# Kernel tuning notes

Hardware: AMD Instinct MI355X
Metric: run time of the kernel (lower is better)

Reference implementation:

```python
import jax, jax.numpy as jnp
import numpy as np

# GNB per-element parameters [s, beta, R, C6] indexed by atomic number Z (rows not listed stay zero)
_ROWS = {
 1:[0.2772,1.7504,3.6516,95.99], 2:[0.2425,2.087,2.1843,40.67], 3:[0.3266,2.3073,1.2711,70.21],
 4:[0.3964,2.8811,3.3497,114.51], 5:[0.3121,2.6366,2.7079,152.36], 6:[0.2455,3.0189,1.8219,184.28],
 7:[0.2743,2.9432,2.4667,482.54], 8:[0.2577,2.7407,2.365,405.57], 9:[0.2791,2.5863,1.5062,218.45],
 10:[0.2378,2.5307,1.8233,174.81], 11:[0.2592,2.5679,1.3974,181.7], 12:[0.3837,2.9613,3.3515,263.02],
 13:[0.3013,3.2377,3.0102,228.1], 14:[0.3202,3.2749,3.1629,359.43], 15:[0.3399,3.7491,3.2554,3222.12],
 16:[0.3215,3.6718,2.9539,2144.49], 17:[0.3071,3.418,3.0368,2072.46], 18:[0.2752,3.3306,2.6598,1357.42],
 19:[0.2264,2.9736,4.0877,1406.65], 20:[0.4015,3.4464,4.1275,1058.36], 21:[0.9388,4.5955,9.7282,11498.73],
 22:[0.6048,3.5334,8.5322,3361.33], 23:[0.3678,3.068,7.2344,2095.91], 24:[0.2848,2.8393,5.3605,1049.31],
 25:[0.355,3.055,3.718,966.27], 26:[0.4406,3.2628,3.6408,1571.36], 27:[0.4124,3.2622,3.4961,1183.59],
 28:[0.3139,2.749,3.5108,787.76], 29:[0.3345,2.9097,3.0537,563.93], 30:[0.3391,2.9024,3.0261,592.91],
 31:[0.3146,3.3924,3.1735,430.82], 32:[0.3327,3.2804,3.1773,812.57], 33:[0.404,3.8757,3.8357,4533.53],
 34:[0.3343,3.8562,3.1109,3440.92], 35:[0.3242,3.7067,3.2122,3859.82], 36:[0.292,3.6457,2.8263,2729.6],
 37:[0.2677,3.4421,2.412,1864.19], 38:[0.3446,3.559,1.894,1175.73], 39:[1.0038,5.7293,11.2061,32141.18],
 40:[0.6146,5.075,6.821,27655.14], 41:[0.4244,3.7156,7.2367,2864.2], 42:[0.4882,3.6853,3.901,3563.45],
 43:[0.4439,3.6987,4.0857,3266.43], 44:[0.4736,3.7826,4.045,3967.23], 45:[0.4039,3.4706,3.4813,2233.82],
 46:[0.3188,3.3433,3.0487,1393.49], 47:[0.2948,3.1186,2.7795,1315.09], 48:[0.3012,3.0853,2.8673,1311.47],
 49:[0.3351,3.5452,3.3339,1460.56], 50:[0.3134,3.2997,3.0086,1662.99], 51:[0.4081,4.1277,3.9919,8089.97],
 52:[0.3585,4.1795,3.4209,6887.05], 53:[0.3574,4.0988,3.5649,8799.32], 54:[0.3134,4.0387,3.0288,6136.5],
 55:[0.2872,3.8468,2.262,3757.31], 56:[0.3788,4.0368,1.3837,2561.18], 57:[1.0851,6.1365,12.171,66580.83],
 72:[0.5577,5.213,6.0791,27593.76], 73:[0.5308,4.7637,5.7661,15364.65], 74:[0.3926,3.6018,3.6366,2734.5],
 75:[0.5351,3.9552,4.241,4801.82], 76:[0.4701,4.0278,4.1348,5685.94], 77:[0.3661,3.6123,3.4213,2786.0],
 78:[0.3411,3.6066,3.2486,2699.79], 79:[0.3164,3.3822,2.9588,2282.6], 80:[0.3047,3.375,2.9381,2476.79],
 81:[0.2802,3.3964,2.7711,2988.7], 82:[0.2682,3.2481,2.5816,2506.63], 83:[0.3876,4.1225,3.785,8916.84],
 84:[0.3679,4.2313,3.5381,8694.22], 85:[0.368,4.2455,3.6985,11821.61], 86:[0.3195,4.1784,3.0551,8410.64],
}
_TAB = np.zeros((87, 4), np.float32)
for _z, _v in _ROWS.items():
    _TAB[_z] = _v
GNB_TABLE = jnp.asarray(_TAB)
C_SP2 = jnp.asarray(np.array([0.2808, 3.0548, 2.2348, 429.69], np.float32))
C_SP3 = jnp.asarray(np.array([0.2455, 3.0189, 1.8219, 184.28], np.float32))
N_CN2 = jnp.asarray(np.array([0.2996, 3.02, 2.6454, 720.18], np.float32))
N_CN3 = jnp.asarray(np.array([0.2743, 2.9432, 2.4667, 482.54], np.float32))

BJ_A1, BJ_A2, BJ_ALPHA = 0.4, 4.0, 14.0
CUTOFF_LR, CUTOFF_START = 10.0, 8.0  # cutoff_start = cutoff_lr - 2.0


def _poly_envelope(x):
    # PolynomialCutoff.calculate_envelope with r_max=1, p=6:
    x6 = x ** 6
    env = 1.0 - 28.0 * x6 + 48.0 * x6 * x - 21.0 * x6 * x * x
    return env * (x < 1.0)


def _gnb_forward(lengths, Z, edge_index):
    n_nodes = Z.shape[0]
    sender, receiver = edge_index[0], edge_index[1]

    # coordination numbers via scatter-add on receiver
    cn = jnp.zeros((n_nodes,), jnp.int32).at[receiver].add(1)

    # species-indexed params with CN-adaptive selection for C and N
    params = GNB_TABLE[Z]  # [N, 4]
    c_params = jnp.where((cn <= 3)[:, None], C_SP2[None, :], C_SP3[None, :])
    n_params = jnp.where((cn <= 2)[:, None], N_CN2[None, :], N_CN3[None, :])
    params = jnp.where((Z == 6)[:, None], c_params, params)
    params = jnp.where((Z == 7)[:, None], n_params, params)

    R_i = params[:, 2]
    C6_i = params[:, 3]

    # geometric-mean combination rules per edge
    C6_ij = jnp.sqrt(C6_i[sender] * C6_i[receiver])
    R_ij = jnp.sqrt(R_i[sender] * R_i[receiver])

    r = lengths
    # BJ damping: f = 1 / (1 + 6 (r/r0)^(-alpha)), r0 = a1 sqrt(R_ij) + a2
    r0 = BJ_A1 * jnp.sqrt(R_ij) + BJ_A2
    f_damp = 1.0 / (1.0 + 6.0 * (r0 / r) ** BJ_ALPHA)

    e_edge = -C6_ij / (R_ij ** 6 + r ** 6) * f_damp

    # long-range polynomial cutoff switching from 1 at cutoff_start to 0 at cutoff_lr
    x = (r - CUTOFF_START) / (CUTOFF_LR - CUTOFF_START)
    env = jnp.where(r < CUTOFF_START, 1.0, _poly_envelope(x))
    e_edge = e_edge * env

    # scatter-sum to atoms; 0.5 to split symmetric pair energy over both directions
    node_energy = jnp.zeros((n_nodes,), e_edge.dtype).at[receiver].add(0.5 * e_edge)
    return node_energy


def setup_inputs() -> dict:
    key = jax.random.key(0)
    k1, k2, k3 = jax.random.split(key, 3)
    n_nodes, n_edges = 100000, 6400000
    Z = jax.random.randint(k1, (n_nodes,), 1, 87, dtype=jnp.int32)
    edge_index = jax.random.randint(k2, (2, n_edges), 0, n_nodes, dtype=jnp.int32)
    lengths = jax.random.uniform(k3, (n_edges,), jnp.float32, 1.0, 10.5)
    return {"Z": Z, "edge_index": edge_index, "lengths": lengths}


def reference(Z, edge_index, lengths):
    return _gnb_forward(lengths, Z, edge_index)
```

## Files before the change

### kernel.cpp

```cpp
#include <hip/hip_runtime.h>


#define B2SHIFT 10
#define B2SIZE  1024
#define TILE    4096
#define SBLK    512
#define ESLICES 32
#define MAXB    128

__device__ __constant__ float2 GNB_RC6[87] = {
    {0.f, 0.f},
    {3.6516f, 95.99f},   {2.1843f, 40.67f},   {1.2711f, 70.21f},
    {3.3497f, 114.51f},  {2.7079f, 152.36f},  {1.8219f, 184.28f},
    {2.4667f, 482.54f},  {2.365f, 405.57f},   {1.5062f, 218.45f},
    {1.8233f, 174.81f},  {1.3974f, 181.7f},   {3.3515f, 263.02f},
    {3.0102f, 228.1f},   {3.1629f, 359.43f},  {3.2554f, 3222.12f},
    {2.9539f, 2144.49f}, {3.0368f, 2072.46f}, {2.6598f, 1357.42f},
    {4.0877f, 1406.65f}, {4.1275f, 1058.36f}, {9.7282f, 11498.73f},
    {8.5322f, 3361.33f}, {7.2344f, 2095.91f}, {5.3605f, 1049.31f},
    {3.718f, 966.27f},   {3.6408f, 1571.36f}, {3.4961f, 1183.59f},
    {3.5108f, 787.76f},  {3.0537f, 563.93f},  {3.0261f, 592.91f},
    {3.1735f, 430.82f},  {3.1773f, 812.57f},  {3.8357f, 4533.53f},
    {3.1109f, 3440.92f}, {3.2122f, 3859.82f}, {2.8263f, 2729.6f},
    {2.412f, 1864.19f},  {1.894f, 1175.73f},  {11.2061f, 32141.18f},
    {6.821f, 27655.14f}, {7.2367f, 2864.2f},  {3.901f, 3563.45f},
    {4.0857f, 3266.43f}, {4.045f, 3967.23f},  {3.4813f, 2233.82f},
    {3.0487f, 1393.49f}, {2.7795f, 1315.09f}, {2.8673f, 1311.47f},
    {3.3339f, 1460.56f}, {3.0086f, 1662.99f}, {3.9919f, 8089.97f},
    {3.4209f, 6887.05f}, {3.5649f, 8799.32f}, {3.0288f, 6136.5f},
    {2.262f, 3757.31f},  {1.3837f, 2561.18f}, {12.171f, 66580.83f},
    {0.f,0.f},{0.f,0.f},{0.f,0.f},{0.f,0.f},{0.f,0.f},{0.f,0.f},{0.f,0.f},
    {0.f,0.f},{0.f,0.f},{0.f,0.f},{0.f,0.f},{0.f,0.f},{0.f,0.f},{0.f,0.f},
    {6.0791f, 27593.76f}, {5.7661f, 15364.65f}, {3.6366f, 2734.5f},
    {4.241f, 4801.82f},   {4.1348f, 5685.94f},  {3.4213f, 2786.0f},
    {3.2486f, 2699.79f},  {2.9588f, 2282.6f},   {2.9381f, 2476.79f},
    {2.7711f, 2988.7f},   {2.5816f, 2506.63f},  {3.785f, 8916.84f},
    {3.5381f, 8694.22f},  {3.6985f, 11821.61f}, {3.0551f, 8410.64f},
};

__global__ void gnb_init(const int* __restrict__ Z, unsigned* __restrict__ isCN,
                         int nw, int n_nodes, int* __restrict__ zp, int zwords) {
    int stride = gridDim.x * blockDim.x;
    int t0 = blockIdx.x * blockDim.x + threadIdx.x;
    for (int i = t0; i < zwords; i += stride) zp[i] = 0;
    for (int w = t0; w < nw; w += stride) {
        unsigned m = 0;
        int base = w << 5;
        int lim = n_nodes - base; if (lim > 32) lim = 32;
        for (int k = 0; k < lim; ++k) {
            int z = Z[base + k];
            if (z == 6 || z == 7) m |= (1u << k);
        }
        isCN[w] = m;
    }
}

__global__ void __launch_bounds__(SBLK)
gnb_scatter(const int* __restrict__ send, const int* __restrict__ recv,
            const float* __restrict__ len, const unsigned* __restrict__ isCN,
            int* __restrict__ cn,
            uint2* __restrict__ buckets, unsigned* __restrict__ cursor,
            uint4* __restrict__ ovrec, unsigned* __restrict__ ocur,
            int n_edges, int cap, unsigned ocap, int NB2) {
    __shared__ unsigned cnt[MAXB];
    __shared__ unsigned pos[MAXB];
    __shared__ unsigned startp[MAXB + 1];
    __shared__ unsigned gbase[MAXB];
    __shared__ uint2 srec[TILE];
    __shared__ unsigned char bmap[TILE];
    const int tid = threadIdx.x;
    const int e0  = blockIdx.x * TILE;

    for (int b = tid; b < MAXB; b += SBLK) { cnt[b] = 0; pos[b] = 0; }
    __syncthreads();

    #pragma unroll
    for (int k = 0; k < 2; ++k) {
        int base = e0 + (k * SBLK + tid) * 4;
        if (base + 3 < n_edges) {
            int4   rv = *(const int4*)(recv + base);
            float4 lv = *(const float4*)(len + base);
            int rr[4] = {rv.x, rv.y, rv.z, rv.w};
            float ll[4] = {lv.x, lv.y, lv.z, lv.w};
            #pragma unroll
            for (int j = 0; j < 4; ++j) {
                unsigned r = (unsigned)rr[j];
                if (ll[j] < 10.0f) atomicAdd(&cnt[r >> B2SHIFT], 1u);
                if ((isCN[r >> 5] >> (r & 31)) & 1u) atomicAdd(&cn[r], 1);
            }
        } else {
            int lim = n_edges - base; if (lim < 0) lim = 0; if (lim > 4) lim = 4;
            for (int j = 0; j < lim; ++j) {
                unsigned r = (unsigned)recv[base + j];
                if (len[base + j] < 10.0f) atomicAdd(&cnt[r >> B2SHIFT], 1u);
                if ((isCN[r >> 5] >> (r & 31)) & 1u) atomicAdd(&cn[r], 1);
            }
        }
    }
    __syncthreads();

    if (tid == 0) {
        unsigned acc = 0;
        for (int b = 0; b < NB2; ++b) { startp[b] = acc; acc += cnt[b]; }
        startp[NB2] = acc;
    }
    __syncthreads();
    if (tid < NB2) gbase[tid] = atomicAdd(&cursor[tid], cnt[tid]);
    __syncthreads();

    #pragma unroll
    for (int k = 0; k < 2; ++k) {
        int base = e0 + (k * SBLK + tid) * 4;
        if (base + 3 < n_edges) {
            int4   sv = *(const int4*)(send + base);
            int4   rv = *(const int4*)(recv + base);
            uint4  lv = *(const uint4*)(len + base);
            int ss[4] = {sv.x, sv.y, sv.z, sv.w};
            int rr[4] = {rv.x, rv.y, rv.z, rv.w};
            unsigned ll[4] = {lv.x, lv.y, lv.z, lv.w};
            #pragma unroll
            for (int j = 0; j < 4; ++j) {
                if (__uint_as_float(ll[j]) >= 10.0f) continue;
                unsigned r = (unsigned)rr[j];
                unsigned b = r >> B2SHIFT;
                unsigned slot = startp[b] + atomicAdd(&pos[b], 1u);
                srec[slot] = make_uint2((unsigned)ss[j] | ((r & (B2SIZE - 1)) << 17), ll[j]);
                bmap[slot] = (unsigned char)b;
            }
        } else {
            int lim = n_edges - base; if (lim < 0) lim = 0; if (lim > 4) lim = 4;
            for (int j = 0; j < lim; ++j) {
                unsigned lbits = ((const unsigned*)len)[base + j];
                if (__uint_as_float(lbits) >= 10.0f) continue;
                unsigned r = (unsigned)recv[base + j];
                unsigned b = r >> B2SHIFT;
                unsigned slot = startp[b] + atomicAdd(&pos[b], 1u);
                srec[slot] = make_uint2((unsigned)send[base + j] | ((r & (B2SIZE - 1)) << 17),
                                        lbits);
                bmap[slot] = (unsigned char)b;
            }
        }
    }
    __syncthreads();

    unsigned total = startp[NB2];
    for (unsigned i = tid; i < total; i += SBLK) {
        unsigned b = bmap[i];
        unsigned g = gbase[b] + (i - startp[b]);
        uint2 rec = srec[i];
        if (g < (unsigned)cap) {
            buckets[(size_t)b * cap + g] = rec;
        } else {
            unsigned o = atomicAdd(ocur, 1u);
            unsigned r = ((unsigned)b << B2SHIFT) | ((rec.x >> 17) & (B2SIZE - 1));
            if (o < ocap) ovrec[o] = make_uint4(r, rec.x & 0x1FFFFu, rec.y, 0u);
        }
    }
}

__global__ void gnb_params(const int* __restrict__ Z, const int* __restrict__ cn,
                           float2* __restrict__ P2, int n_nodes) {
    int i = blockIdx.x * blockDim.x + threadIdx.x;
    if (i >= n_nodes) return;
    int z = Z[i];
    float Rp, C6;
    if (z == 6) {
        if (cn[i] <= 3) { Rp = 2.2348f; C6 = 429.69f; }
        else            { Rp = 1.8219f; C6 = 184.28f; }
    } else if (z == 7) {
        if (cn[i] <= 2) { Rp = 2.6454f; C6 = 720.18f; }
        else            { Rp = 2.4667f; C6 = 482.54f; }
    } else {
        float2 rc = GNB_RC6[z];
        Rp = rc.x; C6 = rc.y;
    }
    P2[i] = make_float2(sqrtf(C6), sqrtf(sqrtf(Rp)));
}

__device__ __forceinline__ float gnb_energy_eval(float2 ps, float2 pr, float rlen) {
    float env;
    if (rlen < 8.0f) {
        env = 1.0f;
    } else {
        float x = (rlen - 8.0f) * 0.5f;
        float x2 = x * x;
        float x6 = x2 * x2 * x2;
        env = 1.0f - 28.0f * x6 + 48.0f * x6 * x - 21.0f * x6 * x2;
    }
    float sR  = ps.y * pr.y;
    float C6  = ps.x * pr.x;
    float Rij = sR * sR;
    float R3  = Rij * Rij * Rij;
    float R6  = R3 * R3;
    float r0  = 0.4f * sR + 4.0f;
    float t   = r0 / rlen;
    float t2 = t * t, t4 = t2 * t2, t8 = t4 * t4;
    float t14 = t8 * t4 * t2;
    float fd = 1.0f / (1.0f + 6.0f * t14);
    float rl2 = rlen * rlen;
    float r6 = rl2 * rl2 * rl2;
    return -0.5f * C6 / (R6 + r6) * fd * env;
}

__global__ void __launch_bounds__(256)
gnb_energy(const uint2* __restrict__ buckets, const unsigned* __restrict__ cursor,
           const float2* __restrict__ P2, float* __restrict__ rep,
           int cap, int n_nodes) {
    __shared__ float  acc[2][B2SIZE + 8];
    __shared__ float2 p2loc[B2SIZE];
    const int b   = blockIdx.x / ESLICES;
    const int sl  = blockIdx.x % ESLICES;
    const int tid = threadIdx.x;
    const int rr  = (tid >> 6) & 1;

    for (int i = tid; i < 2 * (B2SIZE + 8); i += 256) acc[0][i] = 0.0f;
    for (int i = tid; i < B2SIZE; i += 256) {
        int node = (b << B2SHIFT) + i;
        p2loc[i] = (node < n_nodes) ? P2[node] : make_float2(0.f, 0.f);
    }
    __syncthreads();

    unsigned count = cursor[b];
    if (count > (unsigned)cap) count = (unsigned)cap;
    unsigned seg = (count + ESLICES - 1) / ESLICES;
    unsigned st  = (unsigned)sl * seg;
    unsigned en  = st + seg; if (en > count) en = count;

    const uint2* src = buckets + (size_t)b * cap;
    for (unsigned i = st + tid; i < en; i += 256) {
        uint2 rec = src[i];
        unsigned s    = rec.x & 0x1FFFFu;
        unsigned rlow = (rec.x >> 17) & (B2SIZE - 1);
        float e = gnb_energy_eval(P2[s], p2loc[rlow], __uint_as_float(rec.y));
        atomicAdd(&acc[rr][rlow], e);
    }
    __syncthreads();

    float* dst = rep + (size_t)blockIdx.x * B2SIZE;
    for (int i = tid; i < B2SIZE; i += 256) dst[i] = acc[0][i] + acc[1][i];
}

__global__ void gnb_ovf_energy(const uint4* __restrict__ ovrec, const unsigned* __restrict__ ocur,
                               const float2* __restrict__ P2, float* __restrict__ ovf,
                               unsigned ocap) {
    unsigned n = *ocur; if (n > ocap) n = ocap;
    int stride = gridDim.x * blockDim.x;
    for (unsigned i = blockIdx.x * blockDim.x + threadIdx.x; i < n; i += stride) {
        uint4 rec = ovrec[i];
        float rlen = __uint_as_float(rec.z);
        if (rlen >= 10.0f) continue;
        float e = gnb_energy_eval(P2[rec.y], P2[rec.x], rlen);
        atomicAdd(&ovf[rec.x], e);
    }
}

__global__ void gnb_reduce(const float* __restrict__ rep, const float* __restrict__ ovf,
                           float* __restrict__ out, int n_nodes) {
    int i = blockIdx.x * blockDim.x + threadIdx.x;
    if (i >= n_nodes) return;
    int b = i >> B2SHIFT;
    int j = i & (B2SIZE - 1);
    const float* src = rep + ((size_t)b * ESLICES) * B2SIZE + j;
    float sum = ovf[i];
    #pragma unroll
    for (int s = 0; s < ESLICES; ++s) sum += src[(size_t)s * B2SIZE];
    out[i] = sum;
}

extern "C" void kernel_launch(void* const* d_in, const int* in_sizes, int n_in,
                              void* d_out, int out_size, void* d_ws, size_t ws_size,
                              hipStream_t stream) {
    const int*   Z    = (const int*)d_in[0];
    const int*   eidx = (const int*)d_in[1];
    const float* len  = (const float*)d_in[2];
    float*       out  = (float*)d_out;

    const int n_nodes = in_sizes[0];
    const int n_edges = in_sizes[2];
    const int* send = eidx;
    const int* recv = eidx + n_edges;

    const int NB2 = (n_nodes + B2SIZE - 1) >> B2SHIFT;
    const int nw  = (n_nodes + 31) >> 5;
    const int nwp = (nw + 7) & ~7;

    char* ws = (char*)d_ws;
    unsigned* cursor = (unsigned*)ws;
    unsigned* ocur   = (unsigned*)(ws + MAXB * 4);
    int*      cn     = (int*)(ws + (MAXB + 8) * 4);
    float*    ovf    = (float*)(ws + ((size_t)n_nodes + MAXB + 8) * 4);
    float2*   P2     = (float2*)(ws + ((size_t)2 * n_nodes + MAXB + 8) * 4);
    unsigned* isCN   = (unsigned*)(ws + ((size_t)4 * n_nodes + MAXB + 8) * 4);
    float*    rep    = (float*)((char*)isCN + (size_t)nwp * 4);
    size_t rep_w     = (size_t)NB2 * ESLICES * B2SIZE;
    char*     tail   = (char*)rep + rep_w * 4;

    size_t fixed_words = (size_t)4 * n_nodes + MAXB + 8 + nwp + rep_w;
    size_t total_words = ws_size / 4;
    size_t avail = total_words > fixed_words ? total_words - fixed_words : 0;
    size_t ovw = avail / 32;
    unsigned ocap = (unsigned)(ovw / 4);
    long cap = (long)((avail - ovw) / (2 * (size_t)NB2));
    if (cap > n_edges) cap = n_edges;
    if (cap < 0) cap = 0;
    uint4* ovrec   = (uint4*)tail;
    uint2* buckets = (uint2*)(tail + (size_t)ocap * 16);

    const int B = 256;
    int node_blocks = (n_nodes + B - 1) / B;
    int scat_blocks = (n_edges + TILE - 1) / TILE;
    int zero_words  = 2 * n_nodes + MAXB + 8;

    gnb_init<<<256, B, 0, stream>>>(Z, isCN, nw, n_nodes, (int*)ws, zero_words);
    gnb_scatter<<<scat_blocks, SBLK, 0, stream>>>(send, recv, len, isCN, cn, buckets,
                                                  cursor, ovrec, ocur, n_edges,
                                                  (int)cap, ocap, NB2);
    gnb_params<<<node_blocks, B, 0, stream>>>(Z, cn, P2, n_nodes);
    gnb_energy<<<NB2 * ESLICES, B, 0, stream>>>(buckets, cursor, P2, rep, (int)cap, n_nodes);
    gnb_ovf_energy<<<8, B, 0, stream>>>(ovrec, ocur, P2, ovf, ocap);
    gnb_reduce<<<node_blocks, B, 0, stream>>>(rep, ovf, out, n_nodes);
}
```

Measured before the change: 202.4 us.

## Replace bucketed receiver sort with direct global atomics into replicated outputs

```diff
diff --git a/kernel.cpp b/kernel.cpp
--- a/kernel.cpp
+++ b/kernel.cpp
@@ -1,12 +1,8 @@
 #include <hip/hip_runtime.h>
 
 
-#define B2SHIFT 10
-#define B2SIZE  1024
-#define TILE    4096
-#define SBLK    512
-#define ESLICES 32
-#define MAXB    128
+#define REP 16
+#define EB  256
 
 __device__ __constant__ float2 GNB_RC6[87] = {
     {0.f, 0.f},
@@ -38,11 +34,22 @@
     {3.5381f, 8694.22f},  {3.6985f, 11821.61f}, {3.0551f, 8410.64f},
 };
 
+__device__ __forceinline__ void atomic_fadd(float* p, float v) {
+#if defined(__HIP_PLATFORM_AMD__)
+    unsafeAtomicAdd(p, v);
+#else
+    atomicAdd(p, v);
+#endif
+}
+
 __global__ void gnb_init(const int* __restrict__ Z, unsigned* __restrict__ isCN,
-                         int nw, int n_nodes, int* __restrict__ zp, int zwords) {
+                         int nw, int n_nodes, int4* __restrict__ zp4, int zq,
+                         int* __restrict__ zp, long zwords) {
     int stride = gridDim.x * blockDim.x;
     int t0 = blockIdx.x * blockDim.x + threadIdx.x;
-    for (int i = t0; i < zwords; i += stride) zp[i] = 0;
+    int4 z4 = make_int4(0, 0, 0, 0);
+    for (int i = t0; i < zq; i += stride) zp4[i] = z4;
+    for (long i = (long)zq * 4 + t0; i < zwords; i += stride) zp[i] = 0;
     for (int w = t0; w < nw; w += stride) {
         unsigned m = 0;
         int base = w << 5;
@@ -55,105 +62,25 @@
     }
 }
 
-__global__ void __launch_bounds__(SBLK)
-gnb_scatter(const int* __restrict__ send, const int* __restrict__ recv,
-            const float* __restrict__ len, const unsigned* __restrict__ isCN,
-            int* __restrict__ cn,
-            uint2* __restrict__ buckets, unsigned* __restrict__ cursor,
-            uint4* __restrict__ ovrec, unsigned* __restrict__ ocur,
-            int n_edges, int cap, unsigned ocap, int NB2) {
-    __shared__ unsigned cnt[MAXB];
-    __shared__ unsigned pos[MAXB];
-    __shared__ unsigned startp[MAXB + 1];
-    __shared__ unsigned gbase[MAXB];
-    __shared__ uint2 srec[TILE];
-    __shared__ unsigned char bmap[TILE];
-    const int tid = threadIdx.x;
-    const int e0  = blockIdx.x * TILE;
-
-    for (int b = tid; b < MAXB; b += SBLK) { cnt[b] = 0; pos[b] = 0; }
-    __syncthreads();
-
-    #pragma unroll
-    for (int k = 0; k < 2; ++k) {
-        int base = e0 + (k * SBLK + tid) * 4;
-        if (base + 3 < n_edges) {
-            int4   rv = *(const int4*)(recv + base);
-            float4 lv = *(const float4*)(len + base);
-            int rr[4] = {rv.x, rv.y, rv.z, rv.w};
-            float ll[4] = {lv.x, lv.y, lv.z, lv.w};
-            #pragma unroll
-            for (int j = 0; j < 4; ++j) {
-                unsigned r = (unsigned)rr[j];
-                if (ll[j] < 10.0f) atomicAdd(&cnt[r >> B2SHIFT], 1u);
+__global__ void __launch_bounds__(EB)
+gnb_degree(const int* __restrict__ recv, const unsigned* __restrict__ isCN,
+           int* __restrict__ cn, int n_edges) {
+    int base = (blockIdx.x * EB + threadIdx.x) * 4;
+    if (base + 3 < n_edges) {
+        int4 rv = *(const int4*)(recv + base);
+        int rr[4] = {rv.x, rv.y, rv.z, rv.w};
+        #pragma unroll
+        for (int j = 0; j < 4; ++j) {
+            unsigned r = (unsigned)rr[j];
+            if ((isCN[r >> 5] >> (r & 31)) & 1u) atomicAdd(&cn[r], 1);
+        }
+    } else {
+        for (int j = 0; j < 4; ++j) {
+            int e = base + j;
+            if (e < n_edges) {
+                unsigned r = (unsigned)recv[e];
                 if ((isCN[r >> 5] >> (r & 31)) & 1u) atomicAdd(&cn[r], 1);
             }
-        } else {
-            int lim = n_edges - base; if (lim < 0) lim = 0; if (lim > 4) lim = 4;
-            for (int j = 0; j < lim; ++j) {
-                unsigned r = (unsigned)recv[base + j];
-                if (len[base + j] < 10.0f) atomicAdd(&cnt[r >> B2SHIFT], 1u);
-                if ((isCN[r >> 5] >> (r & 31)) & 1u) atomicAdd(&cn[r], 1);
-            }
-        }
-    }
-    __syncthreads();
-
-    if (tid == 0) {
-        unsigned acc = 0;
-        for (int b = 0; b < NB2; ++b) { startp[b] = acc; acc += cnt[b]; }
-        startp[NB2] = acc;
-    }
-    __syncthreads();
-    if (tid < NB2) gbase[tid] = atomicAdd(&cursor[tid], cnt[tid]);
-    __syncthreads();
-
-    #pragma unroll
-    for (int k = 0; k < 2; ++k) {
-        int base = e0 + (k * SBLK + tid) * 4;
-        if (base + 3 < n_edges) {
-            int4   sv = *(const int4*)(send + base);
-            int4   rv = *(const int4*)(recv + base);
-            uint4  lv = *(const uint4*)(len + base);
-            int ss[4] = {sv.x, sv.y, sv.z, sv.w};
-            int rr[4] = {rv.x, rv.y, rv.z, rv.w};
-            unsigned ll[4] = {lv.x, lv.y, lv.z, lv.w};
-            #pragma unroll
-            for (int j = 0; j < 4; ++j) {
-                if (__uint_as_float(ll[j]) >= 10.0f) continue;
-                unsigned r = (unsigned)rr[j];
-                unsigned b = r >> B2SHIFT;
-                unsigned slot = startp[b] + atomicAdd(&pos[b], 1u);
-                srec[slot] = make_uint2((unsigned)ss[j] | ((r & (B2SIZE - 1)) << 17), ll[j]);
-                bmap[slot] = (unsigned char)b;
-            }
-        } else {
-            int lim = n_edges - base; if (lim < 0) lim = 0; if (lim > 4) lim = 4;
-            for (int j = 0; j < lim; ++j) {
-                unsigned lbits = ((const unsigned*)len)[base + j];
-                if (__uint_as_float(lbits) >= 10.0f) continue;
-                unsigned r = (unsigned)recv[base + j];
-                unsigned b = r >> B2SHIFT;
-                unsigned slot = startp[b] + atomicAdd(&pos[b], 1u);
-                srec[slot] = make_uint2((unsigned)send[base + j] | ((r & (B2SIZE - 1)) << 17),
-                                        lbits);
-                bmap[slot] = (unsigned char)b;
-            }
-        }
-    }
-    __syncthreads();
-
-    unsigned total = startp[NB2];
-    for (unsigned i = tid; i < total; i += SBLK) {
-        unsigned b = bmap[i];
-        unsigned g = gbase[b] + (i - startp[b]);
-        uint2 rec = srec[i];
-        if (g < (unsigned)cap) {
-            buckets[(size_t)b * cap + g] = rec;
-        } else {
-            unsigned o = atomicAdd(ocur, 1u);
-            unsigned r = ((unsigned)b << B2SHIFT) | ((rec.x >> 17) & (B2SIZE - 1));
-            if (o < ocap) ovrec[o] = make_uint4(r, rec.x & 0x1FFFFu, rec.y, 0u);
         }
     }
 }
@@ -202,69 +129,51 @@
     return -0.5f * C6 / (R6 + r6) * fd * env;
 }
 
-__global__ void __launch_bounds__(256)
-gnb_energy(const uint2* __restrict__ buckets, const unsigned* __restrict__ cursor,
-           const float2* __restrict__ P2, float* __restrict__ rep,
-           int cap, int n_nodes) {
-    __shared__ float  acc[2][B2SIZE + 8];
-    __shared__ float2 p2loc[B2SIZE];
-    const int b   = blockIdx.x / ESLICES;
-    const int sl  = blockIdx.x % ESLICES;
-    const int tid = threadIdx.x;
-    const int rr  = (tid >> 6) & 1;
-
-    for (int i = tid; i < 2 * (B2SIZE + 8); i += 256) acc[0][i] = 0.0f;
-    for (int i = tid; i < B2SIZE; i += 256) {
-        int node = (b << B2SHIFT) + i;
-        p2loc[i] = (node < n_nodes) ? P2[node] : make_float2(0.f, 0.f);
-    }
-    __syncthreads();
-
-    unsigned count = cursor[b];
-    if (count > (unsigned)cap) count = (unsigned)cap;
-    unsigned seg = (count + ESLICES - 1) / ESLICES;
-    unsigned st  = (unsigned)sl * seg;
-    unsigned en  = st + seg; if (en > count) en = count;
-
-    const uint2* src = buckets + (size_t)b * cap;
-    for (unsigned i = st + tid; i < en; i += 256) {
-        uint2 rec = src[i];
-        unsigned s    = rec.x & 0x1FFFFu;
-        unsigned rlow = (rec.x >> 17) & (B2SIZE - 1);
-        float e = gnb_energy_eval(P2[s], p2loc[rlow], __uint_as_float(rec.y));
-        atomicAdd(&acc[rr][rlow], e);
-    }
-    __syncthreads();
-
-    float* dst = rep + (size_t)blockIdx.x * B2SIZE;
-    for (int i = tid; i < B2SIZE; i += 256) dst[i] = acc[0][i] + acc[1][i];
-}
-
-__global__ void gnb_ovf_energy(const uint4* __restrict__ ovrec, const unsigned* __restrict__ ocur,
-                               const float2* __restrict__ P2, float* __restrict__ ovf,
-                               unsigned ocap) {
-    unsigned n = *ocur; if (n > ocap) n = ocap;
-    int stride = gridDim.x * blockDim.x;
-    for (unsigned i = blockIdx.x * blockDim.x + threadIdx.x; i < n; i += stride) {
-        uint4 rec = ovrec[i];
-        float rlen = __uint_as_float(rec.z);
-        if (rlen >= 10.0f) continue;
-        float e = gnb_energy_eval(P2[rec.y], P2[rec.x], rlen);
-        atomicAdd(&ovf[rec.x], e);
-    }
-}
-
-__global__ void gnb_reduce(const float* __restrict__ rep, const float* __restrict__ ovf,
-                           float* __restrict__ out, int n_nodes) {
+__global__ void __launch_bounds__(EB)
+gnb_energy(const int* __restrict__ send, const int* __restrict__ recv,
+           const float* __restrict__ len, const float2* __restrict__ P2,
+           float* __restrict__ outrep, int n_edges, int n_nodes) {
+    float* myout = outrep +
+        (size_t)(((blockIdx.x << 2) + (threadIdx.x >> 6)) & (REP - 1)) * n_nodes;
+    int base = (blockIdx.x * EB + threadIdx.x) * 4;
+    if (base + 3 < n_edges) {
+        int4   sv = *(const int4*)(send + base);
+        int4   rv = *(const int4*)(recv + base);
+        float4 lv = *(const float4*)(len + base);
+        int ss[4] = {sv.x, sv.y, sv.z, sv.w};
+        int rr[4] = {rv.x, rv.y, rv.z, rv.w};
+        float ll[4] = {lv.x, lv.y, lv.z, lv.w};
+        #pragma unroll
+        for (int j = 0; j < 4; ++j) {
+            if (ll[j] < 10.0f) {
+                float2 ps = P2[ss[j]];
+                float2 pr = P2[rr[j]];
+                float e = gnb_energy_eval(ps, pr, ll[j]);
+                atomic_fadd(&myout[rr[j]], e);
+            }
+        }
+    } else {
+        for (int j = 0; j < 4; ++j) {
+            int e = base + j;
+            if (e < n_edges) {
+                float l = len[e];
+                if (l < 10.0f) {
+                    float en = gnb_energy_eval(P2[send[e]], P2[recv[e]], l);
+                    atomic_fadd(&myout[recv[e]], en);
+                }
+            }
+        }
+    }
+}
+
+__global__ void gnb_reduce(const float* __restrict__ outrep, float* __restrict__ out,
+                           int n_nodes) {
     int i = blockIdx.x * blockDim.x + threadIdx.x;
     if (i >= n_nodes) return;
-    int b = i >> B2SHIFT;
-    int j = i & (B2SIZE - 1);
-    const float* src = rep + ((size_t)b * ESLICES) * B2SIZE + j;
-    float sum = ovf[i];
+    float s = 0.0f;
     #pragma unroll
-    for (int s = 0; s < ESLICES; ++s) sum += src[(size_t)s * B2SIZE];
-    out[i] = sum;
+    for (int rpl = 0; rpl < REP; ++rpl) s += outrep[(size_t)rpl * n_nodes + i];
+    out[i] = s;
 }
 
 extern "C" void kernel_launch(void* const* d_in, const int* in_sizes, int n_in,
@@ -280,43 +189,27 @@
     const int* send = eidx;
     const int* recv = eidx + n_edges;
 
-    const int NB2 = (n_nodes + B2SIZE - 1) >> B2SHIFT;
-    const int nw  = (n_nodes + 31) >> 5;
-    const int nwp = (nw + 7) & ~7;
+    const int nw = (n_nodes + 31) >> 5;
 
     char* ws = (char*)d_ws;
-    unsigned* cursor = (unsigned*)ws;
-    unsigned* ocur   = (unsigned*)(ws + MAXB * 4);
-    int*      cn     = (int*)(ws + (MAXB + 8) * 4);
-    float*    ovf    = (float*)(ws + ((size_t)n_nodes + MAXB + 8) * 4);
-    float2*   P2     = (float2*)(ws + ((size_t)2 * n_nodes + MAXB + 8) * 4);
-    unsigned* isCN   = (unsigned*)(ws + ((size_t)4 * n_nodes + MAXB + 8) * 4);
-    float*    rep    = (float*)((char*)isCN + (size_t)nwp * 4);
-    size_t rep_w     = (size_t)NB2 * ESLICES * B2SIZE;
-    char*     tail   = (char*)rep + rep_w * 4;
-
-    size_t fixed_words = (size_t)4 * n_nodes + MAXB + 8 + nwp + rep_w;
-    size_t total_words = ws_size / 4;
-    size_t avail = total_words > fixed_words ? total_words - fixed_words : 0;
-    size_t ovw = avail / 32;
-    unsigned ocap = (unsigned)(ovw / 4);
-    long cap = (long)((avail - ovw) / (2 * (size_t)NB2));
-    if (cap > n_edges) cap = n_edges;
-    if (cap < 0) cap = 0;
-    uint4* ovrec   = (uint4*)tail;
-    uint2* buckets = (uint2*)(tail + (size_t)ocap * 16);
+    int*      cn     = (int*)ws;
+    float*    outrep = (float*)(ws + (size_t)n_nodes * 4);
+    size_t    p2off  = (((size_t)(1 + REP) * n_nodes) + 1) & ~(size_t)1;
+    float2*   P2     = (float2*)(ws + p2off * 4);
+    unsigned* isCN   = (unsigned*)(ws + (p2off + (size_t)2 * n_nodes) * 4);
+
+    long zwords = (long)(1 + REP) * n_nodes;
+    int  zq     = (int)(zwords / 4);
 
     const int B = 256;
     int node_blocks = (n_nodes + B - 1) / B;
-    int scat_blocks = (n_edges + TILE - 1) / TILE;
-    int zero_words  = 2 * n_nodes + MAXB + 8;
-
-    gnb_init<<<256, B, 0, stream>>>(Z, isCN, nw, n_nodes, (int*)ws, zero_words);
-    gnb_scatter<<<scat_blocks, SBLK, 0, stream>>>(send, recv, len, isCN, cn, buckets,
-                                                  cursor, ovrec, ocur, n_edges,
-                                                  (int)cap, ocap, NB2);
+    int edge_blocks = (n_edges + EB * 4 - 1) / (EB * 4);
+
+    gnb_init<<<256, B, 0, stream>>>(Z, isCN, nw, n_nodes, (int4*)ws, zq,
+                                    (int*)ws, zwords);
+    gnb_degree<<<edge_blocks, EB, 0, stream>>>(recv, isCN, cn, n_edges);
     gnb_params<<<node_blocks, B, 0, stream>>>(Z, cn, P2, n_nodes);
-    gnb_energy<<<NB2 * ESLICES, B, 0, stream>>>(buckets, cursor, P2, rep, (int)cap, n_nodes);
-    gnb_ovf_energy<<<8, B, 0, stream>>>(ovrec, ocur, P2, ovf, ocap);
-    gnb_reduce<<<node_blocks, B, 0, stream>>>(rep, ovf, out, n_nodes);
-}
+    gnb_energy<<<edge_blocks, EB, 0, stream>>>(send, recv, len, P2, outrep,
+                                               n_edges, n_nodes);
+    gnb_reduce<<<node_blocks, B, 0, stream>>>(outrep, out, n_nodes);
+}
```

After: 409.5 us. 2.02x slower.

## Compute edge energies during scatter and bucket energies instead of sender/length records

Applied to the files above, without the earlier changes.

```diff
diff --git a/kernel.cpp b/kernel.cpp
--- a/kernel.cpp
+++ b/kernel.cpp
@@ -5,8 +5,10 @@
 #define B2SIZE  1024
 #define TILE    4096
 #define SBLK    512
+#define NWAVE   8
 #define ESLICES 32
 #define MAXB    128
+#define EB      256
 
 __device__ __constant__ float2 GNB_RC6[87] = {
     {0.f, 0.f},
@@ -38,11 +40,22 @@
     {3.5381f, 8694.22f},  {3.6985f, 11821.61f}, {3.0551f, 8410.64f},
 };
 
+__device__ __forceinline__ void atomic_fadd(float* p, float v) {
+#if defined(__HIP_PLATFORM_AMD__)
+    unsafeAtomicAdd(p, v);
+#else
+    atomicAdd(p, v);
+#endif
+}
+
 __global__ void gnb_init(const int* __restrict__ Z, unsigned* __restrict__ isCN,
-                         int nw, int n_nodes, int* __restrict__ zp, int zwords) {
+                         int nw, int n_nodes, int4* __restrict__ zp4, int zq,
+                         int* __restrict__ zp, int zwords) {
     int stride = gridDim.x * blockDim.x;
     int t0 = blockIdx.x * blockDim.x + threadIdx.x;
-    for (int i = t0; i < zwords; i += stride) zp[i] = 0;
+    int4 z4 = make_int4(0, 0, 0, 0);
+    for (int i = t0; i < zq; i += stride) zp4[i] = z4;
+    for (int i = zq * 4 + t0; i < zwords; i += stride) zp[i] = 0;
     for (int w = t0; w < nw; w += stride) {
         unsigned m = 0;
         int base = w << 5;
@@ -55,105 +68,25 @@
     }
 }
 
-__global__ void __launch_bounds__(SBLK)
-gnb_scatter(const int* __restrict__ send, const int* __restrict__ recv,
-            const float* __restrict__ len, const unsigned* __restrict__ isCN,
-            int* __restrict__ cn,
-            uint2* __restrict__ buckets, unsigned* __restrict__ cursor,
-            uint4* __restrict__ ovrec, unsigned* __restrict__ ocur,
-            int n_edges, int cap, unsigned ocap, int NB2) {
-    __shared__ unsigned cnt[MAXB];
-    __shared__ unsigned pos[MAXB];
-    __shared__ unsigned startp[MAXB + 1];
-    __shared__ unsigned gbase[MAXB];
-    __shared__ uint2 srec[TILE];
-    __shared__ unsigned char bmap[TILE];
-    const int tid = threadIdx.x;
-    const int e0  = blockIdx.x * TILE;
-
-    for (int b = tid; b < MAXB; b += SBLK) { cnt[b] = 0; pos[b] = 0; }
-    __syncthreads();
-
-    #pragma unroll
-    for (int k = 0; k < 2; ++k) {
-        int base = e0 + (k * SBLK + tid) * 4;
-        if (base + 3 < n_edges) {
-            int4   rv = *(const int4*)(recv + base);
-            float4 lv = *(const float4*)(len + base);
-            int rr[4] = {rv.x, rv.y, rv.z, rv.w};
-            float ll[4] = {lv.x, lv.y, lv.z, lv.w};
-            #pragma unroll
-            for (int j = 0; j < 4; ++j) {
-                unsigned r = (unsigned)rr[j];
-                if (ll[j] < 10.0f) atomicAdd(&cnt[r >> B2SHIFT], 1u);
+__global__ void __launch_bounds__(EB)
+gnb_degree(const int* __restrict__ recv, const unsigned* __restrict__ isCN,
+           int* __restrict__ cn, int n_edges) {
+    int base = (blockIdx.x * EB + threadIdx.x) * 4;
+    if (base + 3 < n_edges) {
+        int4 rv = *(const int4*)(recv + base);
+        int rr[4] = {rv.x, rv.y, rv.z, rv.w};
+        #pragma unroll
+        for (int j = 0; j < 4; ++j) {
+            unsigned r = (unsigned)rr[j];
+            if ((isCN[r >> 5] >> (r & 31)) & 1u) atomicAdd(&cn[r], 1);
+        }
+    } else {
+        for (int j = 0; j < 4; ++j) {
+            int e = base + j;
+            if (e < n_edges) {
+                unsigned r = (unsigned)recv[e];
                 if ((isCN[r >> 5] >> (r & 31)) & 1u) atomicAdd(&cn[r], 1);
             }
-        } else {
-            int lim = n_edges - base; if (lim < 0) lim = 0; if (lim > 4) lim = 4;
-            for (int j = 0; j < lim; ++j) {
-                unsigned r = (unsigned)recv[base + j];
-                if (len[base + j] < 10.0f) atomicAdd(&cnt[r >> B2SHIFT], 1u);
-                if ((isCN[r >> 5] >> (r & 31)) & 1u) atomicAdd(&cn[r], 1);
-            }
-        }
-    }
-    __syncthreads();
-
-    if (tid == 0) {
-        unsigned acc = 0;
-        for (int b = 0; b < NB2; ++b) { startp[b] = acc; acc += cnt[b]; }
-        startp[NB2] = acc;
-    }
-    __syncthreads();
-    if (tid < NB2) gbase[tid] = atomicAdd(&cursor[tid], cnt[tid]);
-    __syncthreads();
-
-    #pragma unroll
-    for (int k = 0; k < 2; ++k) {
-        int base = e0 + (k * SBLK + tid) * 4;
-        if (base + 3 < n_edges) {
-            int4   sv = *(const int4*)(send + base);
-            int4   rv = *(const int4*)(recv + base);
-            uint4  lv = *(const uint4*)(len + base);
-            int ss[4] = {sv.x, sv.y, sv.z, sv.w};
-            int rr[4] = {rv.x, rv.y, rv.z, rv.w};
-            unsigned ll[4] = {lv.x, lv.y, lv.z, lv.w};
-            #pragma unroll
-            for (int j = 0; j < 4; ++j) {
-                if (__uint_as_float(ll[j]) >= 10.0f) continue;
-                unsigned r = (unsigned)rr[j];
-                unsigned b = r >> B2SHIFT;
-                unsigned slot = startp[b] + atomicAdd(&pos[b], 1u);
-                srec[slot] = make_uint2((unsigned)ss[j] | ((r & (B2SIZE - 1)) << 17), ll[j]);
-                bmap[slot] = (unsigned char)b;
-            }
-        } else {
-            int lim = n_edges - base; if (lim < 0) lim = 0; if (lim > 4) lim = 4;
-            for (int j = 0; j < lim; ++j) {
-                unsigned lbits = ((const unsigned*)len)[base + j];
-                if (__uint_as_float(lbits) >= 10.0f) continue;
-                unsigned r = (unsigned)recv[base + j];
-                unsigned b = r >> B2SHIFT;
-                unsigned slot = startp[b] + atomicAdd(&pos[b], 1u);
-                srec[slot] = make_uint2((unsigned)send[base + j] | ((r & (B2SIZE - 1)) << 17),
-                                        lbits);
-                bmap[slot] = (unsigned char)b;
-            }
-        }
-    }
-    __syncthreads();
-
-    unsigned total = startp[NB2];
-    for (unsigned i = tid; i < total; i += SBLK) {
-        unsigned b = bmap[i];
-        unsigned g = gbase[b] + (i - startp[b]);
-        uint2 rec = srec[i];
-        if (g < (unsigned)cap) {
-            buckets[(size_t)b * cap + g] = rec;
-        } else {
-            unsigned o = atomicAdd(ocur, 1u);
-            unsigned r = ((unsigned)b << B2SHIFT) | ((rec.x >> 17) & (B2SIZE - 1));
-            if (o < ocap) ovrec[o] = make_uint4(r, rec.x & 0x1FFFFu, rec.y, 0u);
         }
     }
 }
@@ -202,22 +135,138 @@
     return -0.5f * C6 / (R6 + r6) * fd * env;
 }
 
+__global__ void __launch_bounds__(SBLK)
+gnb_scatter(const int* __restrict__ send, const int* __restrict__ recv,
+            const float* __restrict__ len, const float2* __restrict__ P2,
+            uint2* __restrict__ buckets, unsigned* __restrict__ cursor,
+            uint2* __restrict__ ovrec, unsigned* __restrict__ ocur,
+            int n_edges, int cap, unsigned ocap, int NB2) {
+    __shared__ unsigned hist[NWAVE][MAXB];
+    __shared__ unsigned waveBase[NWAVE][MAXB];
+    __shared__ unsigned cntS[MAXB];
+    __shared__ unsigned startp[MAXB + 1];
+    __shared__ unsigned gbase[MAXB];
+    __shared__ uint2 srec[TILE];
+    __shared__ unsigned char bmap[TILE];
+    const int tid = threadIdx.x;
+    const int w   = tid >> 6;
+    const int e0  = blockIdx.x * TILE;
+
+    for (int i = tid; i < NWAVE * MAXB; i += SBLK) (&hist[0][0])[i] = 0;
+    __syncthreads();
+
+    unsigned pk[2][4];
+    float    ev[2][4];
+    const bool full = (e0 + TILE <= n_edges);
+    #pragma unroll
+    for (int k = 0; k < 2; ++k) {
+        int base = e0 + (k * SBLK + tid) * 4;
+        int ss[4]; int rr[4]; float ll[4];
+        if (full) {
+            int4   sv = *(const int4*)(send + base);
+            int4   rv = *(const int4*)(recv + base);
+            float4 lv = *(const float4*)(len + base);
+            ss[0]=sv.x; ss[1]=sv.y; ss[2]=sv.z; ss[3]=sv.w;
+            rr[0]=rv.x; rr[1]=rv.y; rr[2]=rv.z; rr[3]=rv.w;
+            ll[0]=lv.x; ll[1]=lv.y; ll[2]=lv.z; ll[3]=lv.w;
+        } else {
+            for (int j = 0; j < 4; ++j) {
+                int e = base + j;
+                bool ok = (e < n_edges);
+                ss[j] = ok ? send[e] : 0;
+                rr[j] = ok ? recv[e] : 0;
+                ll[j] = ok ? len[e]  : 1.0e9f;
+            }
+        }
+        #pragma unroll
+        for (int j = 0; j < 4; ++j) {
+            if (ll[j] < 10.0f) {
+                float2 ps = P2[ss[j]];
+                float2 pr = P2[rr[j]];
+                ev[k][j] = gnb_energy_eval(ps, pr, ll[j]);
+                unsigned r = (unsigned)rr[j];
+                unsigned b = r >> B2SHIFT;
+                unsigned off = atomicAdd(&hist[w][b], 1u);
+                pk[k][j] = b | ((r & (B2SIZE - 1)) << 7) | (off << 17);
+            } else {
+                pk[k][j] = 0xFFFFFFFFu;
+            }
+        }
+    }
+    __syncthreads();
+
+    if (tid < MAXB) {
+        unsigned acc = 0;
+        #pragma unroll
+        for (int ww = 0; ww < NWAVE; ++ww) {
+            waveBase[ww][tid] = acc;
+            acc += hist[ww][tid];
+        }
+        cntS[tid] = acc;
+    }
+    __syncthreads();
+    if (tid < 64) {
+        unsigned a0 = cntS[2 * tid], a1 = cntS[2 * tid + 1];
+        unsigned s = a0 + a1;
+        unsigned sc = s;
+        #pragma unroll
+        for (int d = 1; d < 64; d <<= 1) {
+            unsigned t = __shfl_up(sc, d);
+            if (tid >= d) sc += t;
+        }
+        unsigned excl = sc - s;
+        startp[2 * tid]     = excl;
+        startp[2 * tid + 1] = excl + a0;
+        if (tid == 63) startp[MAXB] = sc;
+    }
+    __syncthreads();
+    if (tid < NB2) {
+        unsigned c = cntS[tid];
+        gbase[tid] = c ? atomicAdd(&cursor[tid], c) : 0u;
+    }
+    __syncthreads();
+
+    #pragma unroll
+    for (int k = 0; k < 2; ++k) {
+        #pragma unroll
+        for (int j = 0; j < 4; ++j) {
+            unsigned p = pk[k][j];
+            if (p != 0xFFFFFFFFu) {
+                unsigned b    = p & (MAXB - 1);
+                unsigned rlow = (p >> 7) & (B2SIZE - 1);
+                unsigned off  = p >> 17;
+                unsigned slot = startp[b] + waveBase[w][b] + off;
+                srec[slot] = make_uint2(rlow, __float_as_uint(ev[k][j]));
+                bmap[slot] = (unsigned char)b;
+            }
+        }
+    }
+    __syncthreads();
+
+    unsigned total = startp[MAXB];
+    for (unsigned i = tid; i < total; i += SBLK) {
+        unsigned b = bmap[i];
+        unsigned g = gbase[b] + (i - startp[b]);
+        uint2 rec = srec[i];
+        if (g < (unsigned)cap) {
+            buckets[(size_t)b * cap + g] = rec;
+        } else {
+            unsigned o = atomicAdd(ocur, 1u);
+            if (o < ocap) ovrec[o] = make_uint2((b << B2SHIFT) | rec.x, rec.y);
+        }
+    }
+}
+
 __global__ void __launch_bounds__(256)
-gnb_energy(const uint2* __restrict__ buckets, const unsigned* __restrict__ cursor,
-           const float2* __restrict__ P2, float* __restrict__ rep,
-           int cap, int n_nodes) {
-    __shared__ float  acc[2][B2SIZE + 8];
-    __shared__ float2 p2loc[B2SIZE];
+gnb_accum(const uint2* __restrict__ buckets, const unsigned* __restrict__ cursor,
+          float* __restrict__ rep, int cap) {
+    __shared__ float acc[2][B2SIZE + 8];
     const int b   = blockIdx.x / ESLICES;
     const int sl  = blockIdx.x % ESLICES;
     const int tid = threadIdx.x;
     const int rr  = (tid >> 6) & 1;
 
     for (int i = tid; i < 2 * (B2SIZE + 8); i += 256) acc[0][i] = 0.0f;
-    for (int i = tid; i < B2SIZE; i += 256) {
-        int node = (b << B2SHIFT) + i;
-        p2loc[i] = (node < n_nodes) ? P2[node] : make_float2(0.f, 0.f);
-    }
     __syncthreads();
 
     unsigned count = cursor[b];
@@ -229,10 +278,7 @@
     const uint2* src = buckets + (size_t)b * cap;
     for (unsigned i = st + tid; i < en; i += 256) {
         uint2 rec = src[i];
-        unsigned s    = rec.x & 0x1FFFFu;
-        unsigned rlow = (rec.x >> 17) & (B2SIZE - 1);
-        float e = gnb_energy_eval(P2[s], p2loc[rlow], __uint_as_float(rec.y));
-        atomicAdd(&acc[rr][rlow], e);
+        atomicAdd(&acc[rr][rec.x], __uint_as_float(rec.y));
     }
     __syncthreads();
 
@@ -240,17 +286,14 @@
     for (int i = tid; i < B2SIZE; i += 256) dst[i] = acc[0][i] + acc[1][i];
 }
 
-__global__ void gnb_ovf_energy(const uint4* __restrict__ ovrec, const unsigned* __restrict__ ocur,
-                               const float2* __restrict__ P2, float* __restrict__ ovf,
-                               unsigned ocap) {
+__global__ void gnb_ovf_energy(const uint2* __restrict__ ovrec,
+                               const unsigned* __restrict__ ocur,
+                               float* __restrict__ ovf, unsigned ocap) {
     unsigned n = *ocur; if (n > ocap) n = ocap;
     int stride = gridDim.x * blockDim.x;
     for (unsigned i = blockIdx.x * blockDim.x + threadIdx.x; i < n; i += stride) {
-        uint4 rec = ovrec[i];
-        float rlen = __uint_as_float(rec.z);
-        if (rlen >= 10.0f) continue;
-        float e = gnb_energy_eval(P2[rec.y], P2[rec.x], rlen);
-        atomicAdd(&ovf[rec.x], e);
+        uint2 rec = ovrec[i];
+        atomic_fadd(&ovf[rec.x], __uint_as_float(rec.y));
     }
 }
 
@@ -299,24 +342,28 @@
     size_t total_words = ws_size / 4;
     size_t avail = total_words > fixed_words ? total_words - fixed_words : 0;
     size_t ovw = avail / 32;
-    unsigned ocap = (unsigned)(ovw / 4);
+    unsigned ocap = (unsigned)(ovw / 2);
     long cap = (long)((avail - ovw) / (2 * (size_t)NB2));
     if (cap > n_edges) cap = n_edges;
     if (cap < 0) cap = 0;
-    uint4* ovrec   = (uint4*)tail;
-    uint2* buckets = (uint2*)(tail + (size_t)ocap * 16);
+    uint2* ovrec   = (uint2*)tail;
+    uint2* buckets = (uint2*)(tail + (size_t)ocap * 8);
 
     const int B = 256;
     int node_blocks = (n_nodes + B - 1) / B;
+    int edge4_blocks = (n_edges + EB * 4 - 1) / (EB * 4);
     int scat_blocks = (n_edges + TILE - 1) / TILE;
     int zero_words  = 2 * n_nodes + MAXB + 8;
-
-    gnb_init<<<256, B, 0, stream>>>(Z, isCN, nw, n_nodes, (int*)ws, zero_words);
-    gnb_scatter<<<scat_blocks, SBLK, 0, stream>>>(send, recv, len, isCN, cn, buckets,
+    int zq = zero_words / 4;
+
+    gnb_init<<<256, B, 0, stream>>>(Z, isCN, nw, n_nodes, (int4*)ws, zq,
+                                    (int*)ws, zero_words);
+    gnb_degree<<<edge4_blocks, EB, 0, stream>>>(recv, isCN, cn, n_edges);
+    gnb_params<<<node_blocks, B, 0, stream>>>(Z, cn, P2, n_nodes);
+    gnb_scatter<<<scat_blocks, SBLK, 0, stream>>>(send, recv, len, P2, buckets,
                                                   cursor, ovrec, ocur, n_edges,
                                                   (int)cap, ocap, NB2);
-    gnb_params<<<node_blocks, B, 0, stream>>>(Z, cn, P2, n_nodes);
-    gnb_energy<<<NB2 * ESLICES, B, 0, stream>>>(buckets, cursor, P2, rep, (int)cap, n_nodes);
-    gnb_ovf_energy<<<8, B, 0, stream>>>(ovrec, ocur, P2, ovf, ocap);
+    gnb_accum<<<NB2 * ESLICES, B, 0, stream>>>(buckets, cursor, rep, (int)cap);
+    gnb_ovf_energy<<<8, B, 0, stream>>>(ovrec, ocur, ovf, ocap);
     gnb_reduce<<<node_blocks, B, 0, stream>>>(rep, ovf, out, n_nodes);
 }
```

New measurement: 228.6 us. 12.9% more time.
